# Optimization experiments

Measured on AMD Instinct MI355X. Metric: run time of the kernel, lower is better.

The kernel has to match this reference:

```python
import jax, jax.numpy as jnp
import numpy as np

POINT_SIZE = 1000000
LOC_DIM = 16
TIM_DIM = 16
POS_DIM = 32
INPUT_DIM = 5
HID = 32
EPS = 1e-5


def _linear(x, W, b):
    return x @ W.T + b


def _resnet(x, W1, b1, W2, b2):
    # Sequential(ReLU, Linear, ReLU, Linear, Dropout(eval=identity)); out = x + 0.3*net(x)
    h = jax.nn.relu(x)
    h = _linear(h, W1, b1)
    h = jax.nn.relu(h)
    h = _linear(h, W2, b2)
    return x + 0.3 * h


def _chain(x, rW1, rb1, rW2, rb2, W, b):
    for i in range(2):  # two ResNet blocks (fixed, structural)
        x = _resnet(x, rW1[i], rb1[i], rW2[i], rb2[i])
    return _linear(x, W, b)


def _mk_linear(key, out_dim, in_dim):
    k1, k2 = jax.random.split(key)
    s = 1.0 / np.sqrt(in_dim)
    W = jax.random.uniform(k1, (out_dim, in_dim), jnp.float32, -s, s)
    b = jax.random.uniform(k2, (out_dim,), jnp.float32, -s, s)
    return W, b


def _mk_res_stack(key, dim, n=2):
    ks = jax.random.split(key, 4 * n)
    W1s, b1s, W2s, b2s = [], [], [], []
    for i in range(n):
        W1, b1 = _mk_linear(ks[4 * i], dim, dim)
        W2, b2 = _mk_linear(ks[4 * i + 1], dim, dim)
        W1s.append(W1); b1s.append(b1); W2s.append(W2); b2s.append(b2)
    return jnp.stack(W1s), jnp.stack(b1s), jnp.stack(W2s), jnp.stack(b2s)


def setup_inputs() -> dict:
    key = jax.random.key(0)
    ks = iter(jax.random.split(key, 40))
    d = {}
    d["x"] = jax.random.randint(next(ks), (3,), 0, 24, dtype=jnp.int64 if jax.config.jax_enable_x64 else jnp.int32)
    d["hidden"] = jnp.zeros((1, 1, HID), jnp.float32)
    d["pos"] = 3
    # embeddings
    d["loc_emb"] = jax.random.normal(next(ks), (POINT_SIZE, LOC_DIM), jnp.float32)
    d["arr_emb"] = jax.random.normal(next(ks), (24, TIM_DIM), jnp.float32)
    d["dur_emb"] = jax.random.normal(next(ks), (24, TIM_DIM), jnp.float32)
    d["pos_emb"] = jax.random.normal(next(ks), (10, POS_DIM), jnp.float32)
    for name, dim in (("fc1", LOC_DIM), ("fc2", TIM_DIM), ("fc3", TIM_DIM)):
        rW1, rb1, rW2, rb2 = _mk_res_stack(next(ks), dim)
        W, b = _mk_linear(next(ks), INPUT_DIM, dim)
        d[f"{name}_rW1"], d[f"{name}_rb1"], d[f"{name}_rW2"], d[f"{name}_rb2"] = rW1, rb1, rW2, rb2
        d[f"{name}_W"], d[f"{name}_b"] = W, b
    # LayerNorm(15)
    d["ln_g"] = jnp.ones((3 * INPUT_DIM,), jnp.float32)
    d["ln_b"] = jnp.zeros((3 * INPUT_DIM,), jnp.float32)
    # ODE: Linear(5->32) + ResNet(32)
    d["ode_W"], d["ode_b"] = _mk_linear(next(ks), HID, INPUT_DIM)
    oW1, ob1, oW2, ob2 = _mk_res_stack(next(ks), HID, n=1)
    d["ode_rW1"], d["ode_rb1"], d["ode_rW2"], d["ode_rb2"] = oW1[0], ob1[0], oW2[0], ob2[0]
    # heads
    d["fc4_W"], d["fc4_b"] = _mk_linear(next(ks), POINT_SIZE, HID)
    d["fc5_W"], d["fc5_b"] = _mk_linear(next(ks), 24, HID)
    d["fc6_W"], d["fc6_b"] = _mk_linear(next(ks), 24, HID)
    # GRU (input 15, hidden 32)
    d["gru_Wih"], d["gru_bih"] = _mk_linear(next(ks), 3 * HID, 3 * INPUT_DIM)
    d["gru_Whh"], d["gru_bhh"] = _mk_linear(next(ks), 3 * HID, HID)
    return d


def reference(x, hidden, pos, loc_emb, arr_emb, dur_emb, pos_emb,
              fc1_rW1, fc1_rb1, fc1_rW2, fc1_rb2, fc1_W, fc1_b,
              fc2_rW1, fc2_rb1, fc2_rW2, fc2_rb2, fc2_W, fc2_b,
              fc3_rW1, fc3_rb1, fc3_rW2, fc3_rb2, fc3_W, fc3_b,
              ln_g, ln_b, ode_W, ode_b, ode_rW1, ode_rb1, ode_rW2, ode_rb2,
              fc4_W, fc4_b, fc5_W, fc5_b, fc6_W, fc6_b,
              gru_Wih, gru_bih, gru_Whh, gru_bhh):
    pos_e = pos_emb[pos]                                   # (32,)
    loc = _chain(loc_emb[x[0]], fc1_rW1, fc1_rb1, fc1_rW2, fc1_rb2, fc1_W, fc1_b)  # (5,)
    arr = _chain(arr_emb[x[1]], fc2_rW1, fc2_rb1, fc2_rW2, fc2_rb2, fc2_W, fc2_b)  # (5,)
    dur = _chain(dur_emb[x[2]], fc3_rW1, fc3_rb1, fc3_rW2, fc3_rb2, fc3_W, fc3_b)  # (5,)
    point = jnp.concatenate([loc, arr, dur])               # (15,)
    mu = jnp.mean(point)
    var = jnp.mean((point - mu) ** 2)
    point = (point - mu) * jax.lax.rsqrt(var + EPS) * ln_g + ln_b
    # hidden = hidden + ODE(dur)
    ode = _linear(dur, ode_W, ode_b)
    ode = _resnet(ode, ode_rW1, ode_rb1, ode_rW2, ode_rb2)
    h = hidden.reshape(-1) + ode                           # (32,)
    # single GRU step
    gi = gru_Wih @ point + gru_bih
    gh = gru_Whh @ h + gru_bhh
    i_r, i_z, i_n = jnp.split(gi, 3)
    h_r, h_z, h_n = jnp.split(gh, 3)
    r = jax.nn.sigmoid(i_r + h_r)
    z = jax.nn.sigmoid(i_z + h_z)
    n = jnp.tanh(i_n + r * h_n)
    h_new = (1.0 - z) * n + z * h                          # (32,) == out == new hidden
    next_loc = jax.nn.log_softmax(h_new @ fc4_W.T + fc4_b)
    next_arr = jax.nn.log_softmax((h_new + pos_e) @ fc5_W.T + fc5_b)
    next_dur = jax.nn.log_softmax(h_new @ fc6_W.T + fc6_b)
    return (next_loc, next_arr, next_dur, h_new.reshape(1, 1, HID))
```

## Files before the change

kernel.cpp:

```cpp
#include <hip/hip_runtime.h>
#include <math.h>

#define ROWS 1000000
#define NBLK_A 2048
#define NTHR 256
#define TOTAL (NBLK_A * NTHR)
#define NBLK_B 977

struct Params {
    const int*   x; const float* hidden; const int* pos;
    const float* loc_emb; const float* arr_emb; const float* dur_emb; const float* pos_emb;
    const float* f1rW1; const float* f1rb1; const float* f1rW2; const float* f1rb2;
    const float* f1W;   const float* f1b;
    const float* f2rW1; const float* f2rb1; const float* f2rW2; const float* f2rb2;
    const float* f2W;   const float* f2b;
    const float* f3rW1; const float* f3rb1; const float* f3rW2; const float* f3rb2;
    const float* f3W;   const float* f3b;
    const float* ln_g;  const float* ln_b;
    const float* ode_W; const float* ode_b;
    const float* oW1;   const float* ob1; const float* oW2; const float* ob2;
    const float* fc4_W; const float* fc4_b;
    const float* fc5_W; const float* fc5_b;
    const float* fc6_W; const float* fc6_b;
    const float* gWih;  const float* gbih; const float* gWhh; const float* gbhh;
    float* out; float* ws;
};

__global__ __launch_bounds__(NTHR) void bigkernel(Params p)
{
    const int t   = threadIdx.x;
    const int bid = blockIdx.x;
    const int gid = bid * NTHR + t;
    const float4* W4 = (const float4*)p.fc4_W;

    float4 a0[8];
    #pragma unroll
    for (int j = 0; j < 8; ++j) a0[j] = W4[(size_t)gid * 8 + j];
    float b0 = p.fc4_b[gid];

    __shared__ float e[3][16], tr[3][16], h1[3][16];
    __shared__ float praw[15], pnorm[15];
    __shared__ float ode0[32], odt[32], hvec[32], hnew[32], pe[32];
    __shared__ float gi[96], gh[96];
    __shared__ float a5[24], a6[24];
    __shared__ float red[4];

    if (t < 48) {
        int c = t >> 4, j = t & 15;
        const float* emb = (c == 0) ? (p.loc_emb + (size_t)p.x[0] * 16)
                         : (c == 1) ? (p.arr_emb + (size_t)p.x[1] * 16)
                                    : (p.dur_emb + (size_t)p.x[2] * 16);
        e[c][j] = emb[j];
    }
    if (t < 32) pe[t] = p.pos_emb[p.pos[0] * 32 + t];
    __syncthreads();

    for (int i = 0; i < 2; ++i) {
        if (t < 48) { int c = t >> 4, j = t & 15; tr[c][j] = fmaxf(e[c][j], 0.f); }
        __syncthreads();
        if (t < 48) {
            int c = t >> 4, j = t & 15;
            const float* W1 = ((c == 0) ? p.f1rW1 : (c == 1) ? p.f2rW1 : p.f3rW1) + i * 256 + j * 16;
            const float* b1 = ((c == 0) ? p.f1rb1 : (c == 1) ? p.f2rb1 : p.f3rb1) + i * 16;
            float a = b1[j];
            #pragma unroll
            for (int k = 0; k < 16; ++k) a += W1[k] * tr[c][k];
            h1[c][j] = fmaxf(a, 0.f);
        }
        __syncthreads();
        if (t < 48) {
            int c = t >> 4, j = t & 15;
            const float* W2 = ((c == 0) ? p.f1rW2 : (c == 1) ? p.f2rW2 : p.f3rW2) + i * 256 + j * 16;
            const float* b2 = ((c == 0) ? p.f1rb2 : (c == 1) ? p.f2rb2 : p.f3rb2) + i * 16;
            float a = b2[j];
            #pragma unroll
            for (int k = 0; k < 16; ++k) a += W2[k] * h1[c][k];
            e[c][j] += 0.3f * a;
        }
        __syncthreads();
    }

    if (t < 15) {
        int c = t / 5, q = t % 5;
        const float* W = ((c == 0) ? p.f1W : (c == 1) ? p.f2W : p.f3W) + q * 16;
        const float* b = ((c == 0) ? p.f1b : (c == 1) ? p.f2b : p.f3b);
        float a = b[q];
        #pragma unroll
        for (int k = 0; k < 16; ++k) a += W[k] * e[c][k];
        praw[t] = a;
    }
    __syncthreads();

    if (t == 0) {
        float mu = 0.f;
        for (int k = 0; k < 15; ++k) mu += praw[k];
        mu *= (1.f / 15.f);
        float var = 0.f;
        for (int k = 0; k < 15; ++k) { float d = praw[k] - mu; var += d * d; }
        var *= (1.f / 15.f);
        red[0] = mu;
        red[1] = rsqrtf(var + 1e-5f);
    }
    __syncthreads();
    if (t < 15) pnorm[t] = (praw[t] - red[0]) * red[1] * p.ln_g[t] + p.ln_b[t];
    if (t < 32) {
        float a = p.ode_b[t];
        const float* W = p.ode_W + t * 5;
        #pragma unroll
        for (int k = 0; k < 5; ++k) a += W[k] * praw[10 + k];
        ode0[t] = a;
    }
    __syncthreads();
    if (t < 32) {
        float a = p.ob1[t];
        const float* W = p.oW1 + t * 32;
        #pragma unroll
        for (int k = 0; k < 32; ++k) a += W[k] * fmaxf(ode0[k], 0.f);
        odt[t] = fmaxf(a, 0.f);
    }
    __syncthreads();
    if (t < 32) {
        float a = p.ob2[t];
        const float* W = p.oW2 + t * 32;
        #pragma unroll
        for (int k = 0; k < 32; ++k) a += W[k] * odt[k];
        hvec[t] = p.hidden[t] + ode0[t] + 0.3f * a;
    }
    __syncthreads();
    if (t < 64) {
        for (int q = t; q < 96; q += 64) {
            float a = p.gbih[q];
            const float* W = p.gWih + q * 15;
            #pragma unroll
            for (int k = 0; k < 15; ++k) a += W[k] * pnorm[k];
            gi[q] = a;
            float c2 = p.gbhh[q];
            const float* V = p.gWhh + q * 32;
            #pragma unroll
            for (int k = 0; k < 32; ++k) c2 += V[k] * hvec[k];
            gh[q] = c2;
        }
    }
    __syncthreads();
    if (t < 32) {
        float r = 1.f / (1.f + expf(-(gi[t] + gh[t])));
        float z = 1.f / (1.f + expf(-(gi[32 + t] + gh[32 + t])));
        float n = tanhf(gi[64 + t] + r * gh[64 + t]);
        float hn = (1.f - z) * n + z * hvec[t];
        hnew[t] = hn;
        if (bid == 0) p.out[ROWS + 48 + t] = hn;
    }
    __syncthreads();
    if (t < 24) {
        float a = p.fc5_b[t];
        const float* W = p.fc5_W + t * 32;
        #pragma unroll
        for (int k = 0; k < 32; ++k) a += W[k] * (hnew[k] + pe[k]);
        a5[t] = a;
        float b = p.fc6_b[t];
        const float* V = p.fc6_W + t * 32;
        #pragma unroll
        for (int k = 0; k < 32; ++k) b += V[k] * hnew[k];
        a6[t] = b;
    }
    __syncthreads();
    if (t == 0) {
        float m = -INFINITY;
        for (int k = 0; k < 24; ++k) m = fmaxf(m, a5[k]);
        float s = 0.f;
        for (int k = 0; k < 24; ++k) s += expf(a5[k] - m);
        red[2] = m + logf(s);
        m = -INFINITY;
        for (int k = 0; k < 24; ++k) m = fmaxf(m, a6[k]);
        s = 0.f;
        for (int k = 0; k < 24; ++k) s += expf(a6[k] - m);
        red[3] = m + logf(s);
    }
    __syncthreads();
    if (bid == 0 && t < 24) {
        p.out[ROWS + t]      = a5[t] - red[2];
        p.out[ROWS + 24 + t] = a6[t] - red[3];
    }

    float hr[32];
    #pragma unroll
    for (int k = 0; k < 32; ++k) hr[k] = hnew[k];

    const int r1 = gid + TOTAL;
    const bool has1 = (r1 < ROWS);

    float4 a1[8];
    if (has1) {
        #pragma unroll
        for (int j = 0; j < 8; ++j) a1[j] = W4[(size_t)r1 * 8 + j];
    }
    float b1v = has1 ? p.fc4_b[r1] : 0.f;

    float acc0 = b0;
    #pragma unroll
    for (int j = 0; j < 8; ++j)
        acc0 += a0[j].x * hr[4*j] + a0[j].y * hr[4*j+1]
              + a0[j].z * hr[4*j+2] + a0[j].w * hr[4*j+3];
    p.out[gid] = acc0;

    float m = acc0, s = 1.f;

    if (has1) {
        float acc1 = b1v;
        #pragma unroll
        for (int j = 0; j < 8; ++j)
            acc1 += a1[j].x * hr[4*j] + a1[j].y * hr[4*j+1]
                  + a1[j].z * hr[4*j+2] + a1[j].w * hr[4*j+3];
        p.out[r1] = acc1;
        if (acc1 > m) { s = s * __expf(m - acc1) + 1.f; m = acc1; }
        else          { s += __expf(acc1 - m); }
    }

    __shared__ float sm[NTHR], ss[NTHR];
    sm[t] = m; ss[t] = s;
    __syncthreads();
    for (int off = NTHR / 2; off > 0; off >>= 1) {
        if (t < off) {
            float m2 = sm[t + off], s2 = ss[t + off];
            float M  = fmaxf(sm[t], m2);
            ss[t] = ss[t] * expf(sm[t] - M) + s2 * expf(m2 - M);
            sm[t] = M;
        }
        __syncthreads();
    }
    if (t == 0) { p.ws[2 * bid] = sm[0]; p.ws[2 * bid + 1] = ss[0]; }
}

__global__ __launch_bounds__(256) void finalize_kernel(
    const float* __restrict__ partials, float* __restrict__ out)
{
    __shared__ float sm[256], ss[256];
    __shared__ float lse_sh;
    const int t = threadIdx.x;

    float fm = -INFINITY, fs = 0.f;
    for (int i = t; i < NBLK_A; i += 256) {
        float m2 = partials[2 * i], s2 = partials[2 * i + 1];
        float M  = fmaxf(fm, m2);
        fs = fs * expf(fm - M) + s2 * expf(m2 - M);
        fm = M;
    }
    sm[t] = fm; ss[t] = fs;
    __syncthreads();
    for (int off = 128; off > 0; off >>= 1) {
        if (t < off) {
            float m2 = sm[t + off], s2 = ss[t + off];
            float M  = fmaxf(sm[t], m2);
            ss[t] = ss[t] * expf(sm[t] - M) + s2 * expf(m2 - M);
            sm[t] = M;
        }
        __syncthreads();
    }
    if (t == 0) lse_sh = sm[0] + logf(ss[0]);
    __syncthreads();
    const float lse = lse_sh;

    const int idx = blockIdx.x * 256 + t;
    if (idx < ROWS / 4) {
        float4* o4 = (float4*)out;
        float4 v = o4[idx];
        v.x -= lse; v.y -= lse; v.z -= lse; v.w -= lse;
        o4[idx] = v;
    }
}

extern "C" void kernel_launch(void* const* d_in, const int* in_sizes, int n_in,
                              void* d_out, int out_size, void* d_ws, size_t ws_size,
                              hipStream_t stream) {
    Params pr;
    pr.x       = (const int*)  d_in[0];
    pr.hidden  = (const float*)d_in[1];
    pr.pos     = (const int*)  d_in[2];
    pr.loc_emb = (const float*)d_in[3];
    pr.arr_emb = (const float*)d_in[4];
    pr.dur_emb = (const float*)d_in[5];
    pr.pos_emb = (const float*)d_in[6];
    pr.f1rW1 = (const float*)d_in[7];
    pr.f1rb1 = (const float*)d_in[8];
    pr.f1rW2 = (const float*)d_in[9];
    pr.f1rb2 = (const float*)d_in[10];
    pr.f1W   = (const float*)d_in[11];
    pr.f1b   = (const float*)d_in[12];
    pr.f2rW1 = (const float*)d_in[13];
    pr.f2rb1 = (const float*)d_in[14];
    pr.f2rW2 = (const float*)d_in[15];
    pr.f2rb2 = (const float*)d_in[16];
    pr.f2W   = (const float*)d_in[17];
    pr.f2b   = (const float*)d_in[18];
    pr.f3rW1 = (const float*)d_in[19];
    pr.f3rb1 = (const float*)d_in[20];
    pr.f3rW2 = (const float*)d_in[21];
    pr.f3rb2 = (const float*)d_in[22];
    pr.f3W   = (const float*)d_in[23];
    pr.f3b   = (const float*)d_in[24];
    pr.ln_g  = (const float*)d_in[25];
    pr.ln_b  = (const float*)d_in[26];
    pr.ode_W = (const float*)d_in[27];
    pr.ode_b = (const float*)d_in[28];
    pr.oW1   = (const float*)d_in[29];
    pr.ob1   = (const float*)d_in[30];
    pr.oW2   = (const float*)d_in[31];
    pr.ob2   = (const float*)d_in[32];
    pr.fc4_W = (const float*)d_in[33];
    pr.fc4_b = (const float*)d_in[34];
    pr.fc5_W = (const float*)d_in[35];
    pr.fc5_b = (const float*)d_in[36];
    pr.fc6_W = (const float*)d_in[37];
    pr.fc6_b = (const float*)d_in[38];
    pr.gWih  = (const float*)d_in[39];
    pr.gbih  = (const float*)d_in[40];
    pr.gWhh  = (const float*)d_in[41];
    pr.gbhh  = (const float*)d_in[42];
    pr.out = (float*)d_out;
    pr.ws  = (float*)d_ws;

    bigkernel<<<NBLK_A, NTHR, 0, stream>>>(pr);
    finalize_kernel<<<NBLK_B, 256, 0, stream>>>((const float*)d_ws, (float*)d_out);
}
```

Measured before the change: 52.72 us.

## Coalesce fc4 weight loads with 8-lane row groups and double-buffered prefetch

Each row's 32-float weight vector is now read by 8 lanes (one float4 each), so a wave's loads are contiguous. The dot product is reduced with xor shuffles. Each wave handles 4 iterations of 64 rows, with the next batch prefetched into a second register buffer while the current one is processed, and the block count is halved, which also halves the redundant per-block preamble. Because all 8 lanes feed the online softmax, each row is counted 8 times; the finalize step corrects this by subtracting ln 8. The trade-off is redundant exp work, a clamped tail load, and more registers held for the two buffers.

```diff
diff --git a/kernel.cpp b/kernel.cpp
--- a/kernel.cpp
+++ b/kernel.cpp
@@ -2,10 +2,13 @@
 #include <math.h>
 
 #define ROWS 1000000
-#define NBLK_A 2048
+#define NBLK_A 1024
 #define NTHR 256
-#define TOTAL (NBLK_A * NTHR)
+#define WAVES 4
+#define GW (NBLK_A * WAVES)
+#define NITER 4
 #define NBLK_B 977
+#define LN8 2.0794415416798357f
 
 struct Params {
     const int*   x; const float* hidden; const int* pos;
@@ -30,13 +33,24 @@
 {
     const int t   = threadIdx.x;
     const int bid = blockIdx.x;
-    const int gid = bid * NTHR + t;
+    const int l   = t & 63;
+    const int wid = t >> 6;
+    const int wg  = bid * WAVES + wid;
+    const int j   = l & 7;
+    const int g   = l >> 3;
     const float4* W4 = (const float4*)p.fc4_W;
 
-    float4 a0[8];
-    #pragma unroll
-    for (int j = 0; j < 8; ++j) a0[j] = W4[(size_t)gid * 8 + j];
-    float b0 = p.fc4_b[gid];
+#define LOADB(dst, it)                                                        \
+    {   _Pragma("unroll")                                                     \
+        for (int c = 0; c < 8; ++c) {                                         \
+            size_t f4 = (size_t)(((it) * GW + wg) * 8 + c) * 64 + l;          \
+            if (f4 >= (size_t)ROWS * 8) f4 = (size_t)ROWS * 8 - 1;            \
+            dst[c] = W4[f4];                                                  \
+        }                                                                     \
+    }
+
+    float4 bA[8], bB[8];
+    LOADB(bA, 0)
 
     __shared__ float e[3][16], tr[3][16], h1[3][16];
     __shared__ float praw[15], pnorm[15];
@@ -46,36 +60,36 @@
     __shared__ float red[4];
 
     if (t < 48) {
-        int c = t >> 4, j = t & 15;
+        int c = t >> 4, jj = t & 15;
         const float* emb = (c == 0) ? (p.loc_emb + (size_t)p.x[0] * 16)
                          : (c == 1) ? (p.arr_emb + (size_t)p.x[1] * 16)
                                     : (p.dur_emb + (size_t)p.x[2] * 16);
-        e[c][j] = emb[j];
+        e[c][jj] = emb[jj];
     }
     if (t < 32) pe[t] = p.pos_emb[p.pos[0] * 32 + t];
     __syncthreads();
 
     for (int i = 0; i < 2; ++i) {
-        if (t < 48) { int c = t >> 4, j = t & 15; tr[c][j] = fmaxf(e[c][j], 0.f); }
+        if (t < 48) { int c = t >> 4, jj = t & 15; tr[c][jj] = fmaxf(e[c][jj], 0.f); }
         __syncthreads();
         if (t < 48) {
-            int c = t >> 4, j = t & 15;
-            const float* W1 = ((c == 0) ? p.f1rW1 : (c == 1) ? p.f2rW1 : p.f3rW1) + i * 256 + j * 16;
+            int c = t >> 4, jj = t & 15;
+            const float* W1 = ((c == 0) ? p.f1rW1 : (c == 1) ? p.f2rW1 : p.f3rW1) + i * 256 + jj * 16;
             const float* b1 = ((c == 0) ? p.f1rb1 : (c == 1) ? p.f2rb1 : p.f3rb1) + i * 16;
-            float a = b1[j];
+            float a = b1[jj];
             #pragma unroll
             for (int k = 0; k < 16; ++k) a += W1[k] * tr[c][k];
-            h1[c][j] = fmaxf(a, 0.f);
+            h1[c][jj] = fmaxf(a, 0.f);
         }
         __syncthreads();
         if (t < 48) {
-            int c = t >> 4, j = t & 15;
-            const float* W2 = ((c == 0) ? p.f1rW2 : (c == 1) ? p.f2rW2 : p.f3rW2) + i * 256 + j * 16;
+            int c = t >> 4, jj = t & 15;
+            const float* W2 = ((c == 0) ? p.f1rW2 : (c == 1) ? p.f2rW2 : p.f3rW2) + i * 256 + jj * 16;
             const float* b2 = ((c == 0) ? p.f1rb2 : (c == 1) ? p.f2rb2 : p.f3rb2) + i * 16;
-            float a = b2[j];
+            float a = b2[jj];
             #pragma unroll
             for (int k = 0; k < 16; ++k) a += W2[k] * h1[c][k];
-            e[c][j] += 0.3f * a;
+            e[c][jj] += 0.3f * a;
         }
         __syncthreads();
     }
@@ -182,39 +196,32 @@
         p.out[ROWS + 24 + t] = a6[t] - red[3];
     }
 
-    float hr[32];
-    #pragma unroll
-    for (int k = 0; k < 32; ++k) hr[k] = hnew[k];
-
-    const int r1 = gid + TOTAL;
-    const bool has1 = (r1 < ROWS);
-
-    float4 a1[8];
-    if (has1) {
-        #pragma unroll
-        for (int j = 0; j < 8; ++j) a1[j] = W4[(size_t)r1 * 8 + j];
-    }
-    float b1v = has1 ? p.fc4_b[r1] : 0.f;
-
-    float acc0 = b0;
-    #pragma unroll
-    for (int j = 0; j < 8; ++j)
-        acc0 += a0[j].x * hr[4*j] + a0[j].y * hr[4*j+1]
-              + a0[j].z * hr[4*j+2] + a0[j].w * hr[4*j+3];
-    p.out[gid] = acc0;
-
-    float m = acc0, s = 1.f;
-
-    if (has1) {
-        float acc1 = b1v;
-        #pragma unroll
-        for (int j = 0; j < 8; ++j)
-            acc1 += a1[j].x * hr[4*j] + a1[j].y * hr[4*j+1]
-                  + a1[j].z * hr[4*j+2] + a1[j].w * hr[4*j+3];
-        p.out[r1] = acc1;
-        if (acc1 > m) { s = s * __expf(m - acc1) + 1.f; m = acc1; }
-        else          { s += __expf(acc1 - m); }
-    }
+    const float h0 = hnew[4 * j], h1v = hnew[4 * j + 1],
+                h2 = hnew[4 * j + 2], h3 = hnew[4 * j + 3];
+    float m = -INFINITY, s = 0.f;
+
+#define PROCESS(src, it)                                                      \
+    {   _Pragma("unroll")                                                     \
+        for (int c = 0; c < 8; ++c) {                                         \
+            float pp = src[c].x * h0 + src[c].y * h1v                         \
+                     + src[c].z * h2 + src[c].w * h3;                         \
+            pp += __shfl_xor(pp, 1);                                          \
+            pp += __shfl_xor(pp, 2);                                          \
+            pp += __shfl_xor(pp, 4);                                          \
+            int row = (((it) * GW + wg) * 8 + c) * 8 + g;                     \
+            if (row < ROWS) {                                                 \
+                float logit = pp + p.fc4_b[row];                              \
+                if (j == 0) p.out[row] = logit;                               \
+                if (logit > m) { s = s * __expf(m - logit) + 1.f; m = logit; }\
+                else           { s += __expf(logit - m); }                    \
+            }                                                                 \
+        }                                                                     \
+    }
+
+    LOADB(bB, 1)  PROCESS(bA, 0)
+    LOADB(bA, 2)  PROCESS(bB, 1)
+    LOADB(bB, 3)  PROCESS(bA, 2)
+                  PROCESS(bB, 3)
 
     __shared__ float sm[NTHR], ss[NTHR];
     sm[t] = m; ss[t] = s;
@@ -256,7 +263,7 @@
         }
         __syncthreads();
     }
-    if (t == 0) lse_sh = sm[0] + logf(ss[0]);
+    if (t == 0) lse_sh = sm[0] + logf(ss[0]) - LN8;
     __syncthreads();
     const float lse = lse_sh;
 
```

After: 48.64 us. 7.7% less time.
